# Kernel tuning notes

Measured on AMD Instinct MI355X. Metric: run time of the kernel, lower is better.

Reference implementation:

```python
import jax, jax.numpy as jnp
import numpy as np

H = 20  # num heads; d_head = 1280 // 20 = 64


def setup_inputs() -> dict:
    key = jax.random.key(0)
    ks = jax.random.split(key, 7)
    B, S, C = 1, 2304, 1280
    hidden_states = jax.random.normal(ks[0], (B, S, C), dtype=jnp.float32)
    # structured boolean sparsity mask (True = keep); force diagonal True so no row is fully masked
    mask = jax.random.randint(ks[1], (S, S), 0, 2) > 0
    mask = mask | jnp.eye(S, dtype=bool)
    w_scale = 0.02  # keep logits in a sane range
    Wq = jax.random.normal(ks[2], (C, C), dtype=jnp.float32) * w_scale
    Wk = jax.random.normal(ks[3], (C, C), dtype=jnp.float32) * w_scale
    Wv = jax.random.normal(ks[4], (C, C), dtype=jnp.float32) * w_scale
    Wo = jax.random.normal(ks[5], (C, C), dtype=jnp.float32) * w_scale
    bo = jnp.zeros((C,), dtype=jnp.float32)
    return {"hidden_states": hidden_states, "mask": mask, "Wq": Wq, "Wk": Wk, "Wv": Wv, "Wo": Wo, "bo": bo}


def reference(hidden_states, mask, Wq, Wk, Wv, Wo, bo):
    B, S, C = hidden_states.shape
    d = C // H
    scale = 1.0 / jnp.sqrt(jnp.float32(d))
    # additive mask: masked_fill(mask == False, -inf)
    add_mask = jnp.where(mask, jnp.float32(0.0), -jnp.inf)  # [S, S]
    # projections (bias-free to_q/to_k/to_v as in diffusers)
    q = hidden_states @ Wq  # [B, S, C]
    k = hidden_states @ Wk
    v = hidden_states @ Wv
    # head_to_batch_dim: [B, S, C] -> [B, H, S, d]
    q = q.reshape(B, S, H, d).transpose(0, 2, 1, 3)
    k = k.reshape(B, S, H, d).transpose(0, 2, 1, 3)
    v = v.reshape(B, S, H, d).transpose(0, 2, 1, 3)
    # get_attention_scores: baddbmm(mask, q, k^T, alpha=scale, beta=1) then softmax
    scores = jnp.einsum("bhqd,bhkd->bhqk", q, k) * scale + add_mask
    probs = jax.nn.softmax(scores, axis=-1)  # [B, H, S, S]
    out = jnp.einsum("bhqk,bhkd->bhqd", probs, v)  # [B, H, S, d]
    # batch_to_head_dim: [B, H, S, d] -> [B, S, C]
    out = out.transpose(0, 2, 1, 3).reshape(B, S, C)
    # to_out[0] Linear + to_out[1] Dropout(eval = identity)
    out = out @ Wo + bo
    return out
```

## Files before the change

kernel.cpp:

```cpp
#include <hip/hip_runtime.h>
#include <stdint.h>

typedef __attribute__((ext_vector_type(8))) short short8;
typedef __attribute__((ext_vector_type(4))) float f32x4;
typedef __attribute__((ext_vector_type(4))) unsigned int u32x4;
typedef unsigned short u16;
typedef unsigned int u32;

#define SEQ  2304
#define CDIM 1280
#define NH   20
#define DH   64
#define MW   72
#define SCL  0.18033688011112043f

__device__ __forceinline__ u16 f2bf(float x){
  u32 u = __builtin_bit_cast(u32, x);
  u += 0x7fffu + ((u >> 16) & 1u);
  return (u16)(u >> 16);
}
__device__ __forceinline__ float bf2f(u16 x){
  u32 u = ((u32)x) << 16;
  return __builtin_bit_cast(float, u);
}

__device__ __forceinline__ u32 cvtpk(float lo, float hi){
  u32 r;
  asm("v_cvt_pk_bf16_f32 %0, %1, %2" : "=v"(r) : "v"(lo), "v"(hi));
  return r;
}

__device__ __forceinline__ void gload16(const void* g, void* l){
  auto gp = (const u32 __attribute__((address_space(1)))*)(uintptr_t)g;
  auto lp = (u32 __attribute__((address_space(3)))*)(uintptr_t)l;
  __builtin_amdgcn_global_load_lds(gp, lp, 16, 0, 0);
}

__global__ __launch_bounds__(256) void k_prep(
    const float* __restrict__ X, const int* __restrict__ Mk,
    const float* __restrict__ w0, const float* __restrict__ w1,
    const float* __restrict__ w2, const float* __restrict__ w3,
    u16* __restrict__ Xb, u32* __restrict__ mb,
    u16* __restrict__ o0, u16* __restrict__ o1,
    u16* __restrict__ o2, u16* __restrict__ o3){
  __shared__ u16 t[64][65];
  int b = blockIdx.x, tid = threadIdx.x;
  if (b < 1440){
    int i = (b*256 + tid)*8;
    float4 v0 = *(const float4*)(X + i);
    float4 v1 = *(const float4*)(X + i + 4);
    short8 o;
    o[0]=(short)f2bf(v0.x); o[1]=(short)f2bf(v0.y); o[2]=(short)f2bf(v0.z); o[3]=(short)f2bf(v0.w);
    o[4]=(short)f2bf(v1.x); o[5]=(short)f2bf(v1.y); o[6]=(short)f2bf(v1.z); o[7]=(short)f2bf(v1.w);
    *(short8*)(Xb + i) = o;
  } else if (b < 3040){
    int b2 = b - 1440;
    int z = b2 / 400, xy = b2 % 400;
    const float* w = z==0?w0: z==1?w1: z==2?w2: w3;
    u16* o        = z==0?o0: z==1?o1: z==2?o2: o3;
    int bx = (xy % 20)*64, by = (xy / 20)*64;
    #pragma unroll
    for (int i = 0; i < 16; i++){
      int idx = tid + i*256; int r = idx>>6, c = idx&63;
      t[r][c] = f2bf(w[(size_t)(by+r)*CDIM + bx + c]);
    }
    __syncthreads();
    #pragma unroll
    for (int i = 0; i < 16; i++){
      int idx = tid + i*256; int r = idx>>6, c = idx&63;
      o[(size_t)(bx+r)*CDIM + by + c] = t[c][r];
    }
  } else {
    int b3 = b - 3040;
    int lane = tid & 63;
    #pragma unroll 4
    for (int it = 0; it < 32; it++){
      int f = (b3*32 + it)*256 + tid;
      unsigned long long bal = __ballot(Mk[f] != 0);
      if ((lane & 31) == 0) mb[f >> 5] = (u32)(bal >> (lane & 32));
    }
  }
}

__global__ __launch_bounds__(256) void k_vt(const u16* __restrict__ v, u16* __restrict__ vt){
  __shared__ u16 t[64][65];
  int bx = blockIdx.x*64, by = blockIdx.y*64, tid = threadIdx.x;
  #pragma unroll
  for (int i = 0; i < 16; i++){
    int idx = tid + i*256; int r = idx>>6, c = idx&63;
    t[r][c] = v[(size_t)(by+r)*CDIM + bx + c];
  }
  if (tid < 64) vt[((size_t)blockIdx.x*80 + 64)*SEQ + by + tid] = 0x3F80;
  __syncthreads();
  #pragma unroll
  for (int i = 0; i < 16; i++){
    int idx = tid + i*256; int r = idx>>6, c = idx&63;
    int s = by + c;
    int x = s & 127;
    int nx = ((x>>5)<<5) | (((x>>2)&3)<<3) | (((x>>4)&1)<<2) | (x&3);
    vt[((size_t)blockIdx.x*80 + r)*SEQ + (s & ~127) + nx] = t[c][r];
  }
}

#define STG(kt, buf) do{ \
  _Pragma("unroll") for (int i = 0; i < 2; i++){ \
    int c = i*256 + w*64 + l; int r = c>>2, gr = c&3, sg = gr ^ ((r>>1)&3); \
    gload16(A + (size_t)(m0+r)*CDIM + (kt)*32 + sg*8, &Al[buf][(i*256 + w*64)*8]); } \
  _Pragma("unroll") for (int i = 0; i < 2; i++){ \
    int c = i*256 + w*64 + l; int r = c>>2, gr = c&3, sg = gr ^ ((r>>1)&3); \
    gload16(B + (size_t)(n0+r)*CDIM + (kt)*32 + sg*8, &Bl[buf][(i*256 + w*64)*8]); } \
}while(0)

template<int EPI>
__global__ __launch_bounds__(256) void k_gemm(const u16* __restrict__ A,
    const u16* __restrict__ B0, const u16* __restrict__ B1, const u16* __restrict__ B2,
    u16* __restrict__ O0, u16* __restrict__ O1, u16* __restrict__ O2,
    float* __restrict__ OF0, float* __restrict__ OF1){
  const u16* B; u16* O = nullptr; float* OP = nullptr;
  int k0, nk;
  if constexpr (EPI == 0){
    B = blockIdx.z==0 ? B0 : blockIdx.z==1 ? B1 : B2;
    O = blockIdx.z==0 ? O0 : blockIdx.z==1 ? O1 : O2;
    k0 = 0; nk = 40;
  } else {
    B = B0; OP = blockIdx.z ? OF1 : OF0;
    k0 = blockIdx.z*20; nk = 20;
  }
  const float qs = (EPI==0 && blockIdx.z==0) ? SCL : 1.0f;
  __shared__ __align__(16) u16 Al[2][128*32];
  __shared__ __align__(16) u16 Bl[2][128*32];
  int tid = threadIdx.x, w = tid>>6, l = tid&63, c16 = l&15, g = l>>4;
  int wr = w>>1, wc = w&1;
  int m0 = blockIdx.y*128, n0 = blockIdx.x*128;
  f32x4 acc[4][4] = {};
  STG(k0, 0);
  __syncthreads();
  int cur = 0;
  for (int kk = 0; kk < nk; ++kk){
    if (kk+1 < nk) STG(k0+kk+1, cur^1);
    short8 af[4], bf[4];
    #pragma unroll
    for (int m = 0; m < 4; m++){
      int r = wr*64 + m*16 + c16; int sg = g ^ ((r>>1)&3);
      af[m] = *(const short8*)&Al[cur][r*32 + sg*8];
    }
    #pragma unroll
    for (int n = 0; n < 4; n++){
      int r = wc*64 + n*16 + c16; int sg = g ^ ((r>>1)&3);
      bf[n] = *(const short8*)&Bl[cur][r*32 + sg*8];
    }
    #pragma unroll
    for (int m = 0; m < 4; m++)
      #pragma unroll
      for (int n = 0; n < 4; n++)
        acc[m][n] = __builtin_amdgcn_mfma_f32_16x16x32_bf16(af[m], bf[n], acc[m][n], 0, 0, 0);
    if (kk+1 < nk){
      __syncthreads();
      cur ^= 1;
    }
  }
  #pragma unroll
  for (int m = 0; m < 4; m++)
    #pragma unroll
    for (int n = 0; n < 4; n++)
      #pragma unroll
      for (int r = 0; r < 4; r++){
        int row = m0 + wr*64 + m*16 + g*4 + r;
        int col = n0 + wc*64 + n*16 + c16;
        float v = acc[m][n][r];
        if constexpr (EPI == 0) O[(size_t)row*CDIM + col] = f2bf(v * qs);
        else                    OP[(size_t)row*CDIM + col] = v;
      }
}

__global__ __launch_bounds__(256) void k_fin(const float* __restrict__ P0, const float* __restrict__ P1,
                                             const float* __restrict__ bias, float* __restrict__ out){
  int i = (blockIdx.x*256 + threadIdx.x)*4;
  int col = i % CDIM;
  float4 a = *(const float4*)(P0 + i);
  float4 b = *(const float4*)(P1 + i);
  float4 c = *(const float4*)(bias + col);
  float4 o = {a.x+b.x+c.x, a.y+b.y+c.y, a.z+b.z+c.z, a.w+b.w+c.w};
  *(float4*)(out + i) = o;
}

__global__ __launch_bounds__(256, 4) void k_attn(const u16* __restrict__ Q, const u16* __restrict__ K,
    const u16* __restrict__ Vt, const u32* __restrict__ mb,
    u16* __restrict__ N0, u16* __restrict__ N1, u16* __restrict__ N2, float* __restrict__ lrb){
  __shared__ __align__(16) u16 Kl[128*64];
  __shared__ __align__(16) u16 Vl[80*128];
  int tid = threadIdx.x, w = tid>>6, l = tid&63, c16 = l&15, g = l>>4;
  int g4 = g*4;
  int q0 = blockIdx.x*64, h = blockIdx.y, z = blockIdx.z;
  short8 qf[2];
  #pragma unroll
  for (int kf = 0; kf < 2; kf++)
    qf[kf] = *(const short8*)&Q[(size_t)(q0 + w*16 + c16)*CDIM + h*DH + kf*32 + g*8];
  const u32* mrow = mb + (size_t)(q0 + w*16 + c16)*MW;
  f32x4 acc[4] = {};
  f32x4 acc5 = {};
  const f32x4 zz = {0.f, 0.f, 0.f, 0.f};
  for (int kt0 = 0; kt0 < 6; ++kt0){
    int kt = z*6 + kt0;
    #pragma unroll
    for (int i = 0; i < 4; i++){
      int c = i*256 + w*64 + l;
      int r = c>>3, gr = c&7, sg = gr ^ (r&7);
      gload16(K + (size_t)(kt*128 + r)*CDIM + h*DH + sg*8, &Kl[(i*256 + w*64)*8]);
    }
    #pragma unroll
    for (int i = 0; i < 5; i++){
      int c = i*256 + w*64 + l;
      int r = c>>4, gr = c&15, sg = gr ^ (r&7);
      gload16(Vt + ((size_t)h*80 + r)*SEQ + kt*128 + sg*8, &Vl[(i*256 + w*64)*8]);
    }
    u32x4 mw4 = *(const u32x4*)(mrow + kt*4);
    __syncthreads();
    f32x4 s[8];
    __builtin_amdgcn_s_setprio(1);
    #pragma unroll
    for (int fj = 0; fj < 8; fj++){
      s[fj] = zz;
      #pragma unroll
      for (int kf = 0; kf < 2; kf++){
        int rk = fj*16 + c16;
        int sg = (kf*4 + g) ^ (rk&7);
        short8 kb = *(const short8*)&Kl[rk*64 + sg*8];
        s[fj] = __builtin_amdgcn_mfma_f32_16x16x32_bf16(kb, qf[kf], s[fj], 0, 0, 0);
      }
    }
    __builtin_amdgcn_s_setprio(0);
    #pragma unroll
    for (int fj = 0; fj < 8; fj++){
      u32 mwsh = mw4[fj>>1] >> (((fj&1)<<4) + g4);
      #pragma unroll
      for (int r = 0; r < 4; r++){
        float sv = (mwsh & (1u<<r)) ? s[fj][r] : -1e30f;
        s[fj][r] = __builtin_exp2f(sv);
      }
    }
    short8 pa[4];
    #pragma unroll
    for (int kf = 0; kf < 4; kf++){
      u32x4 pw;
      pw[0] = cvtpk(s[2*kf  ][0], s[2*kf  ][1]);
      pw[1] = cvtpk(s[2*kf  ][2], s[2*kf  ][3]);
      pw[2] = cvtpk(s[2*kf+1][0], s[2*kf+1][1]);
      pw[3] = cvtpk(s[2*kf+1][2], s[2*kf+1][3]);
      pa[kf] = __builtin_bit_cast(short8, pw);
    }
    __builtin_amdgcn_s_setprio(1);
    #pragma unroll
    for (int fj = 0; fj < 4; fj++)
      #pragma unroll
      for (int kf = 0; kf < 4; kf++){
        int rv = fj*16 + c16;
        int sg = (kf*4 + g) ^ (rv&7);
        short8 vb = *(const short8*)&Vl[rv*128 + sg*8];
        acc[fj] = __builtin_amdgcn_mfma_f32_16x16x32_bf16(pa[kf], vb, acc[fj], 0, 0, 0);
      }
    #pragma unroll
    for (int kf = 0; kf < 4; kf++){
      int rv = 64 + c16;
      int sg = (kf*4 + g) ^ (rv&7);
      short8 vb = *(const short8*)&Vl[rv*128 + sg*8];
      acc5 = __builtin_amdgcn_mfma_f32_16x16x32_bf16(pa[kf], vb, acc5, 0, 0, 0);
    }
    __builtin_amdgcn_s_setprio(0);
    __syncthreads();
  }
  u16* __restrict__ NB = z==0 ? N0 : z==1 ? N1 : N2;
  float inv[4];
  #pragma unroll
  for (int r = 0; r < 4; r++){
    float lrow = __shfl(acc5[r], l & 48);
    inv[r] = lrow > 0.f ? __builtin_amdgcn_rcpf(lrow) : 0.f;
  }
  #pragma unroll
  for (int fj = 0; fj < 4; fj++)
    #pragma unroll
    for (int r = 0; r < 4; r++){
      int row = q0 + w*16 + g4 + r;
      int col = h*DH + fj*16 + c16;
      NB[(size_t)row*CDIM + col] = f2bf(acc[fj][r] * inv[r]);
    }
  if (c16 == 0){
    #pragma unroll
    for (int r = 0; r < 4; r++)
      lrb[((size_t)z*NH + h)*SEQ + q0 + w*16 + g4 + r] = acc5[r];
  }
}

__global__ __launch_bounds__(256) void k_comb(const u16* __restrict__ N0, const u16* __restrict__ N1,
                                              const u16* __restrict__ N2,
                                              const float* __restrict__ lrb, u16* __restrict__ Ab){
  int e = blockIdx.x*256 + threadIdx.x;
  int row = e / 160, c8 = e % 160;
  int h = c8 >> 3;
  float l0 = lrb[(size_t)h*SEQ + row];
  float l1 = lrb[((size_t)NH + h)*SEQ + row];
  float l2 = lrb[((size_t)2*NH + h)*SEQ + row];
  float ws = __builtin_amdgcn_rcpf(l0 + l1 + l2);
  float w0 = l0*ws, w1 = l1*ws, w2 = l2*ws;
  size_t base = (size_t)row*CDIM + c8*8;
  short8 a = *(const short8*)(N0 + base);
  short8 b = *(const short8*)(N1 + base);
  short8 c = *(const short8*)(N2 + base);
  short8 o;
  #pragma unroll
  for (int j = 0; j < 8; j++)
    o[j] = (short)f2bf(bf2f((u16)a[j])*w0 + bf2f((u16)b[j])*w1 + bf2f((u16)c[j])*w2);
  *(short8*)(Ab + base) = o;
}

extern "C" void kernel_launch(void* const* d_in, const int* in_sizes, int n_in,
                              void* d_out, int out_size, void* d_ws, size_t ws_size,
                              hipStream_t stream){
  const float* X  = (const float*)d_in[0];
  const int*   Mk = (const int*)  d_in[1];
  const float* Wq = (const float*)d_in[2];
  const float* Wk = (const float*)d_in[3];
  const float* Wv = (const float*)d_in[4];
  const float* Wo = (const float*)d_in[5];
  const float* bo = (const float*)d_in[6];
  float* out = (float*)d_out;
  char* ws = (char*)d_ws;
  const size_t SZ_XB = (size_t)SEQ*CDIM*2;
  const size_t SZ_WT = (size_t)CDIM*CDIM*2;
  const size_t SZ_VT = (size_t)NH*80*SEQ*2;
  u16* Xb  = (u16*)(ws);
  u16* WqT = (u16*)(ws + SZ_XB);
  u16* WkT = (u16*)(ws + SZ_XB + 1*SZ_WT);
  u16* WvT = (u16*)(ws + SZ_XB + 2*SZ_WT);
  u16* WoT = (u16*)(ws + SZ_XB + 3*SZ_WT);
  u16* Qb  = (u16*)(ws + 1*SZ_XB + 4*SZ_WT);
  u16* Kb  = (u16*)(ws + 2*SZ_XB + 4*SZ_WT);
  u16* Vb  = (u16*)(ws + 3*SZ_XB + 4*SZ_WT);
  u16* Vt  = (u16*)(ws + 4*SZ_XB + 4*SZ_WT);
  u32* mbp = (u32*)(ws + 4*SZ_XB + 4*SZ_WT + SZ_VT);
  float* lrb = (float*)(ws + 4*SZ_XB + 4*SZ_WT + SZ_VT + (size_t)SEQ*MW*4);
  u16* N0 = Vb;
  u16* N1 = Xb;
  u16* N2 = WqT;
  u16* Ab = Vt;
  float* P0 = (float*)Qb;
  float* P1 = (float*)ws;

  k_prep<<<3688, 256, 0, stream>>>(X, Mk, Wq, Wk, Wv, Wo, Xb, mbp, WqT, WkT, WvT, WoT);
  k_gemm<0><<<dim3(10,18,3), 256, 0, stream>>>(Xb, WqT, WkT, WvT, Qb, Kb, Vb, nullptr, nullptr);
  k_vt<<<dim3(20,36), 256, 0, stream>>>(Vb, Vt);
  k_attn<<<dim3(36,20,3), 256, 0, stream>>>(Qb, Kb, Vt, mbp, N0, N1, N2, lrb);
  k_comb<<<1440, 256, 0, stream>>>(N0, N1, N2, lrb, Ab);
  k_gemm<1><<<dim3(10,18,2), 256, 0, stream>>>(Ab, WoT, WoT, WoT, nullptr, nullptr, nullptr, P0, P1);
  k_fin<<<2880, 256, 0, stream>>>(P0, P1, bo, out);
}
```

Before: 245.2 us.

## Remap block IDs per XCD and halve attention key tile to 64

The GEMM and attention kernels now use 1D grids and remap block IDs so that consecutive logical tiles land on the same XCD, aiming for better L2 reuse of shared operands across the chiplets. The attention kernel's key/value tile shrinks from 128 to 64 keys, with 12 iterations instead of 6. That cuts LDS use per block, and launch bounds rise from 4 to 8 blocks per CU to raise occupancy. In exchange it adds more barriers and loop overhead per key, plus smaller MFMA batches between syncs.

```diff
diff --git a/kernel.cpp b/kernel.cpp
--- a/kernel.cpp
+++ b/kernel.cpp
@@ -116,22 +116,30 @@
     const u16* __restrict__ B0, const u16* __restrict__ B1, const u16* __restrict__ B2,
     u16* __restrict__ O0, u16* __restrict__ O1, u16* __restrict__ O2,
     float* __restrict__ OF0, float* __restrict__ OF1){
+  int bid = blockIdx.x, nid;
+  if constexpr (EPI == 0){
+    int xcd = bid & 7, idx = bid >> 3;
+    nid = (xcd < 4 ? xcd*68 : 272 + (xcd-4)*67) + idx;
+  } else {
+    nid = (bid & 7)*45 + (bid >> 3);
+  }
+  int bx = nid % 10, byz = nid / 10, by = byz % 18, bz = byz / 18;
   const u16* B; u16* O = nullptr; float* OP = nullptr;
   int k0, nk;
   if constexpr (EPI == 0){
-    B = blockIdx.z==0 ? B0 : blockIdx.z==1 ? B1 : B2;
-    O = blockIdx.z==0 ? O0 : blockIdx.z==1 ? O1 : O2;
+    B = bz==0 ? B0 : bz==1 ? B1 : B2;
+    O = bz==0 ? O0 : bz==1 ? O1 : O2;
     k0 = 0; nk = 40;
   } else {
-    B = B0; OP = blockIdx.z ? OF1 : OF0;
-    k0 = blockIdx.z*20; nk = 20;
-  }
-  const float qs = (EPI==0 && blockIdx.z==0) ? SCL : 1.0f;
+    B = B0; OP = bz ? OF1 : OF0;
+    k0 = bz*20; nk = 20;
+  }
+  const float qs = (EPI==0 && bz==0) ? SCL : 1.0f;
   __shared__ __align__(16) u16 Al[2][128*32];
   __shared__ __align__(16) u16 Bl[2][128*32];
   int tid = threadIdx.x, w = tid>>6, l = tid&63, c16 = l&15, g = l>>4;
   int wr = w>>1, wc = w&1;
-  int m0 = blockIdx.y*128, n0 = blockIdx.x*128;
+  int m0 = by*128, n0 = bx*128;
   f32x4 acc[4][4] = {};
   STG(k0, 0);
   __syncthreads();
@@ -184,14 +192,17 @@
   *(float4*)(out + i) = o;
 }
 
-__global__ __launch_bounds__(256, 4) void k_attn(const u16* __restrict__ Q, const u16* __restrict__ K,
+__global__ __launch_bounds__(256, 8) void k_attn(const u16* __restrict__ Q, const u16* __restrict__ K,
     const u16* __restrict__ Vt, const u32* __restrict__ mb,
     u16* __restrict__ N0, u16* __restrict__ N1, u16* __restrict__ N2, float* __restrict__ lrb){
-  __shared__ __align__(16) u16 Kl[128*64];
-  __shared__ __align__(16) u16 Vl[80*128];
+  __shared__ __align__(16) u16 Kl[64*64];
+  __shared__ __align__(16) u16 Vl[80*64];
   int tid = threadIdx.x, w = tid>>6, l = tid&63, c16 = l&15, g = l>>4;
   int g4 = g*4;
-  int q0 = blockIdx.x*64, h = blockIdx.y, z = blockIdx.z;
+  int bid = blockIdx.x;
+  int nid = (bid & 7)*270 + (bid >> 3);
+  int qx = nid % 36, hz = nid / 36, h = hz % 20, z = hz / 20;
+  int q0 = qx*64;
   short8 qf[2];
   #pragma unroll
   for (int kf = 0; kf < 2; kf++)
@@ -200,26 +211,28 @@
   f32x4 acc[4] = {};
   f32x4 acc5 = {};
   const f32x4 zz = {0.f, 0.f, 0.f, 0.f};
-  for (int kt0 = 0; kt0 < 6; ++kt0){
-    int kt = z*6 + kt0;
-    #pragma unroll
-    for (int i = 0; i < 4; i++){
+  for (int kt0 = 0; kt0 < 12; ++kt0){
+    int kt = z*12 + kt0;
+    #pragma unroll
+    for (int i = 0; i < 2; i++){
       int c = i*256 + w*64 + l;
       int r = c>>3, gr = c&7, sg = gr ^ (r&7);
-      gload16(K + (size_t)(kt*128 + r)*CDIM + h*DH + sg*8, &Kl[(i*256 + w*64)*8]);
-    }
-    #pragma unroll
-    for (int i = 0; i < 5; i++){
+      gload16(K + (size_t)(kt*64 + r)*CDIM + h*DH + sg*8, &Kl[(i*256 + w*64)*8]);
+    }
+    #pragma unroll
+    for (int i = 0; i < 3; i++){
       int c = i*256 + w*64 + l;
-      int r = c>>4, gr = c&15, sg = gr ^ (r&7);
-      gload16(Vt + ((size_t)h*80 + r)*SEQ + kt*128 + sg*8, &Vl[(i*256 + w*64)*8]);
-    }
-    u32x4 mw4 = *(const u32x4*)(mrow + kt*4);
+      if (c < 520){
+        int r = c>>3, gr = c&7, sg = gr ^ (r&7);
+        gload16(Vt + ((size_t)h*80 + r)*SEQ + kt*64 + sg*8, &Vl[(i*256 + w*64)*8]);
+      }
+    }
+    u32 mw0 = mrow[kt*2], mw1 = mrow[kt*2 + 1];
     __syncthreads();
-    f32x4 s[8];
+    f32x4 s[4];
     __builtin_amdgcn_s_setprio(1);
     #pragma unroll
-    for (int fj = 0; fj < 8; fj++){
+    for (int fj = 0; fj < 4; fj++){
       s[fj] = zz;
       #pragma unroll
       for (int kf = 0; kf < 2; kf++){
@@ -231,17 +244,17 @@
     }
     __builtin_amdgcn_s_setprio(0);
     #pragma unroll
-    for (int fj = 0; fj < 8; fj++){
-      u32 mwsh = mw4[fj>>1] >> (((fj&1)<<4) + g4);
+    for (int fj = 0; fj < 4; fj++){
+      u32 mwsh = (fj < 2 ? mw0 : mw1) >> (((fj&1)<<4) + g4);
       #pragma unroll
       for (int r = 0; r < 4; r++){
         float sv = (mwsh & (1u<<r)) ? s[fj][r] : -1e30f;
         s[fj][r] = __builtin_exp2f(sv);
       }
     }
-    short8 pa[4];
-    #pragma unroll
-    for (int kf = 0; kf < 4; kf++){
+    short8 pa[2];
+    #pragma unroll
+    for (int kf = 0; kf < 2; kf++){
       u32x4 pw;
       pw[0] = cvtpk(s[2*kf  ][0], s[2*kf  ][1]);
       pw[1] = cvtpk(s[2*kf  ][2], s[2*kf  ][3]);
@@ -253,17 +266,17 @@
     #pragma unroll
     for (int fj = 0; fj < 4; fj++)
       #pragma unroll
-      for (int kf = 0; kf < 4; kf++){
+      for (int kf = 0; kf < 2; kf++){
         int rv = fj*16 + c16;
         int sg = (kf*4 + g) ^ (rv&7);
-        short8 vb = *(const short8*)&Vl[rv*128 + sg*8];
+        short8 vb = *(const short8*)&Vl[rv*64 + sg*8];
         acc[fj] = __builtin_amdgcn_mfma_f32_16x16x32_bf16(pa[kf], vb, acc[fj], 0, 0, 0);
       }
     #pragma unroll
-    for (int kf = 0; kf < 4; kf++){
+    for (int kf = 0; kf < 2; kf++){
       int rv = 64 + c16;
       int sg = (kf*4 + g) ^ (rv&7);
-      short8 vb = *(const short8*)&Vl[rv*128 + sg*8];
+      short8 vb = *(const short8*)&Vl[rv*64 + sg*8];
       acc5 = __builtin_amdgcn_mfma_f32_16x16x32_bf16(pa[kf], vb, acc5, 0, 0, 0);
     }
     __builtin_amdgcn_s_setprio(0);
@@ -347,10 +360,10 @@
   float* P1 = (float*)ws;
 
   k_prep<<<3688, 256, 0, stream>>>(X, Mk, Wq, Wk, Wv, Wo, Xb, mbp, WqT, WkT, WvT, WoT);
-  k_gemm<0><<<dim3(10,18,3), 256, 0, stream>>>(Xb, WqT, WkT, WvT, Qb, Kb, Vb, nullptr, nullptr);
+  k_gemm<0><<<540, 256, 0, stream>>>(Xb, WqT, WkT, WvT, Qb, Kb, Vb, nullptr, nullptr);
   k_vt<<<dim3(20,36), 256, 0, stream>>>(Vb, Vt);
-  k_attn<<<dim3(36,20,3), 256, 0, stream>>>(Qb, Kb, Vt, mbp, N0, N1, N2, lrb);
+  k_attn<<<2160, 256, 0, stream>>>(Qb, Kb, Vt, mbp, N0, N1, N2, lrb);
   k_comb<<<1440, 256, 0, stream>>>(N0, N1, N2, lrb, Ab);
-  k_gemm<1><<<dim3(10,18,2), 256, 0, stream>>>(Ab, WoT, WoT, WoT, nullptr, nullptr, nullptr, P0, P1);
+  k_gemm<1><<<360, 256, 0, stream>>>(Ab, WoT, WoT, WoT, nullptr, nullptr, nullptr, P0, P1);
   k_fin<<<2880, 256, 0, stream>>>(P0, P1, bo, out);
 }
```

Result: slower. 269.2 us (+9.8%).
